# Performance work log

Measured on AMD Instinct MI355X. Metric: run time of the kernel, lower is better.

## Reference

```python
import jax, jax.numpy as jnp
import numpy as np

WH, WW = 7, 7
NUM_PRI = 3  # num_priorset=1 -> 3 prior tokens


def _rel_index():
    # Swin relative position index, extended with 3 prior-token columns.
    ch = np.arange(WH)
    cw = np.arange(WW)
    coords = np.stack(np.meshgrid(ch, cw, indexing='ij')).reshape(2, -1)  # [2, N]
    rel = coords[:, :, None] - coords[:, None, :]                          # [2, N, N]
    rel = rel.transpose(1, 2, 0).astype(np.int64)
    rel[..., 0] += WH - 1
    rel[..., 1] += WW - 1
    rel[..., 0] *= 2 * WW - 1
    idx = rel.sum(-1)                                                      # [N, N]
    N = WH * WW
    last = (2 * WH - 1) * (2 * WW - 1)  # 169
    full = np.full((N, N + NUM_PRI), last, dtype=np.int64)
    full[:, :N] = idx
    for j in range(NUM_PRI):
        full[:, N + j] = last + j
    return full

REL_IDX = jnp.asarray(_rel_index())  # [N, N+3]


def setup_inputs() -> dict:
    key = jax.random.key(0)
    ks = jax.random.split(key, 10)
    B, H, W, C = 8, 224, 224, 96
    nW = (H // WH) * (W // WW)  # 1024
    B_ = B * nW                  # 8192
    N = WH * WW                  # 49
    return {
        'x': jax.random.normal(ks[0], (B_, N, C), jnp.float32),
        'mask': jax.random.normal(ks[1], (nW, N, N), jnp.float32),
        'uk_prior': jax.random.normal(ks[2], (B, 1, C), jnp.float32),
        'fg_prior': jax.random.normal(ks[3], (B, 1, C), jnp.float32),
        'bg_prior': jax.random.normal(ks[4], (B, 1, C), jnp.float32),
        'qkv_w': jax.random.normal(ks[5], (3 * C, C), jnp.float32) * 0.02,
        'qkv_b': jax.random.normal(ks[6], (3 * C,), jnp.float32) * 0.02,
        'proj_w': jax.random.normal(ks[7], (C, C), jnp.float32) * 0.02,
        'proj_b': jax.random.normal(ks[8], (C,), jnp.float32) * 0.02,
        'bias_table': jax.random.normal(ks[9], (169 + NUM_PRI, 3), jnp.float32) * 0.02,
        'H': H,
        'W': W,
    }


def reference(x, mask, uk_prior, fg_prior, bg_prior, qkv_w, qkv_b, proj_w, proj_b, bias_table, H, W):
    B_, N, C = x.shape
    nH = bias_table.shape[1]
    hd = C // nH
    scale = hd ** (-0.5)
    nW = (H // WH) * (W // WW)
    B = B_ // nW

    prior_hw = jnp.concatenate([uk_prior, fg_prior, bg_prior], axis=1)  # [B, 3, C]
    # replicate the 3 priors into every window: [B, nW, 3, C] -> [B_, 3, C]
    pri = jnp.broadcast_to(prior_hw[:, None, :, :], (B, nW, NUM_PRI, C)).reshape(B_, NUM_PRI, C)
    x_ext = jnp.concatenate([x, pri], axis=1)                            # [B_, N+3, C]

    qkv = (x_ext @ qkv_w.T + qkv_b).reshape(B_, N + NUM_PRI, 3, nH, hd)
    qkv = qkv.transpose(2, 0, 3, 1, 4)                                   # [3, B_, nH, N+3, hd]
    q, k, v = qkv[0], qkv[1], qkv[2]
    q = q[:, :, :N, :] * scale                                           # [B_, nH, N, hd]

    attn = jnp.einsum('bhnd,bhmd->bhnm', q, k)                           # [B_, nH, N, N+3]
    bias = bias_table[REL_IDX]                                           # [N, N+3, nH]
    attn = attn + bias.transpose(2, 0, 1)[None]

    mask_p = jnp.pad(mask, ((0, 0), (0, 0), (0, NUM_PRI)))               # [nW, N, N+3]
    attn = attn.reshape(B, nW, nH, N, N + NUM_PRI) + mask_p[None, :, None]
    attn = jax.nn.softmax(attn.reshape(B_, nH, N, N + NUM_PRI), axis=-1)

    out = jnp.einsum('bhnm,bhmd->bnhd', attn, v).reshape(B_, N, C)
    out = out @ proj_w.T + proj_b

    # prior highway: run qkv on the raw priors, take v, project
    qkv_hw = (prior_hw @ qkv_w.T + qkv_b).reshape(B, NUM_PRI, 3, nH, hd)
    v_hw = qkv_hw[:, :, 2].reshape(B, NUM_PRI, C)
    v_hw = v_hw @ proj_w.T + proj_b
    return out, v_hw
```

## Files before the change

kernel.cpp:

```cpp
#include <hip/hip_runtime.h>
#include <hip/hip_bf16.h>


typedef __bf16 bf16x8 __attribute__((ext_vector_type(8)));
typedef float  f32x4  __attribute__((ext_vector_type(4)));
typedef short  s16x4  __attribute__((ext_vector_type(4)));
typedef unsigned short u16x4 __attribute__((ext_vector_type(4)));
using bf16 = __hip_bfloat16;

#define SCALE 0.17677669529663687f

#define LDS_XQ    0
#define LDS_K     4900
#define LDS_P     10100
#define LDS_VT    13432
#define LDS_TOT   19960

static __device__ inline float s2f(unsigned short s) {
    unsigned int u = ((unsigned int)s) << 16;
    float f;
    __builtin_memcpy(&f, &u, 4);
    return f;
}
static __device__ inline short f2s(float f) {
    __bf16 h = (__bf16)f;
    short s;
    __builtin_memcpy(&s, &h, 2);
    return s;
}
static __device__ inline bf16x8 ldw8(const float* p) {
    f32x4 a = *reinterpret_cast<const f32x4*>(p);
    f32x4 b = *reinterpret_cast<const f32x4*>(p + 4);
    bf16x8 r;
    #pragma unroll
    for (int i = 0; i < 4; ++i) {
        r[i]     = (__bf16)a[i];
        r[i + 4] = (__bf16)b[i];
    }
    return r;
}

__global__ __launch_bounds__(256)
void pawsa_prep(const float* __restrict__ qkv_w, const float* __restrict__ proj_w,
                const float* __restrict__ bias_table, bf16* __restrict__ ws)
{
    int blk = blockIdx.x, t = threadIdx.x;
    if (blk < 144) {
        int i = blk * 256 + t;
        if (i < 27648)      ws[i] = __float2bfloat16(qkv_w[i]);
        else if (i < 36864) ws[i] = __float2bfloat16(proj_w[i - 27648]);
        return;
    }
    int lane = t & 63, wid = t >> 6;
    int lr = lane & 15, lg = lane >> 4;
    u16x4* bg = reinterpret_cast<u16x4*>(ws + 36864);
    for (int h = 0; h < 3; ++h) {
        for (int nt = 0; nt < 4; ++nt) {
            int c = nt * 16 + lr;
            u16x4 v4;
            for (int j = 0; j < 4; ++j) {
                int n = wid * 16 + lg * 4 + j;
                int idx = 171;
                if (c < 49) {
                    idx = (n / 7 - c / 7 + 6) * 13 + ((n % 7) - (c % 7) + 6);
                    if (idx > 171 || idx < 0) idx = 171;
                } else if (c < 52) {
                    idx = 169 + (c - 49);
                }
                v4[j] = (unsigned short)f2s(bias_table[idx * 3 + h]);
            }
            bg[(h * 4 + nt) * 256 + t] = v4;
        }
    }
}

__global__ __launch_bounds__(256, 4)
void pawsa_main(const float* __restrict__ x, const float* __restrict__ mask,
                const float* __restrict__ uk, const float* __restrict__ fg,
                const float* __restrict__ bg,
                const bf16* __restrict__ wq,
                const float* __restrict__ qkv_b,
                const bf16* __restrict__ wp,
                const float* __restrict__ proj_b,
                const u16x4* __restrict__ biasg,
                float* __restrict__ out)
{
    __shared__ short smem[LDS_TOT];

    const int tid  = threadIdx.x;
    const int bid  = blockIdx.x;
    const int xcd  = bid & 7;
    const int slot = bid >> 3;
    const int wi   = xcd * 128 + (slot & 127);
    const int b    = slot >> 7;
    const int w    = b * 1024 + wi;

    const int lane = tid & 63;
    const int wid  = tid >> 6;
    const int lr   = lane & 15;
    const int lg   = lane >> 4;

    bf16x8 af[3][4];
    #pragma unroll
    for (int mt = 0; mt < 4; ++mt) {
        int n = mt * 16 + lr;
        #pragma unroll
        for (int ks = 0; ks < 3; ++ks) {
            bf16x8 a = (bf16x8)0;
            if (n < 49) {
                a = ldw8(x + ((size_t)w * 49 + n) * 96 + ks * 32 + lg * 8);
            } else if (n < 52) {
                const float* pr = (n == 49) ? uk : (n == 50) ? fg : bg;
                a = ldw8(pr + b * 96 + ks * 32 + lg * 8);
            }
            af[ks][mt] = a;
        }
    }

    const int nt0 = (wid < 3) ? wid * 5 : 13;
    #pragma unroll
    for (int i = 0; i < 5; ++i) {
        int nt = nt0 + i;
        bf16x8 bw0 = *reinterpret_cast<const bf16x8*>(wq + (nt * 16 + lr) * 96 +  0 + lg * 8);
        bf16x8 bw1 = *reinterpret_cast<const bf16x8*>(wq + (nt * 16 + lr) * 96 + 32 + lg * 8);
        bf16x8 bw2 = *reinterpret_cast<const bf16x8*>(wq + (nt * 16 + lr) * 96 + 64 + lg * 8);
        f32x4 qb4 = *reinterpret_cast<const f32x4*>(qkv_b + nt * 16 + lg * 4);
        f32x4 acc[4] = {(f32x4)0.f, (f32x4)0.f, (f32x4)0.f, (f32x4)0.f};
        #pragma unroll
        for (int mt = 0; mt < 4; ++mt) {
            acc[mt] = __builtin_amdgcn_mfma_f32_16x16x32_bf16(bw0, af[0][mt], acc[mt], 0, 0, 0);
            acc[mt] = __builtin_amdgcn_mfma_f32_16x16x32_bf16(bw1, af[1][mt], acc[mt], 0, 0, 0);
            acc[mt] = __builtin_amdgcn_mfma_f32_16x16x32_bf16(bw2, af[2][mt], acc[mt], 0, 0, 0);
        }
        int s = nt / 6;
        int remBase = (nt - s * 6) * 16 + lg * 4;
        #pragma unroll
        for (int mt = 0; mt < 4; ++mt) {
            int n = mt * 16 + lr;
            if (s == 2) {
                #pragma unroll
                for (int j = 0; j < 4; ++j)
                    smem[LDS_VT + (remBase + j) * 68 + n] = f2s(acc[mt][j] + qb4[j]);
            } else {
                s16x4 pk;
                #pragma unroll
                for (int j = 0; j < 4; ++j) pk[j] = f2s(acc[mt][j] + qb4[j]);
                if (s == 0) { if (n < 49) *reinterpret_cast<s16x4*>(
                                  &smem[LDS_XQ + n * 100 + remBase]) = pk; }
                else        { if (n < 52) *reinterpret_cast<s16x4*>(
                                  &smem[LDS_K  + n * 100 + remBase]) = pk; }
            }
        }
    }

    float mk[4][4];
    #pragma unroll
    for (int nt = 0; nt < 4; ++nt) {
        int c = nt * 16 + lr;
        #pragma unroll
        for (int j = 0; j < 4; ++j) {
            int n = wid * 16 + lg * 4 + j;
            float m = 0.f;
            if (c < 49 && n < 49)
                m = mask[(size_t)wi * 2401 + n * 49 + c];
            mk[nt][j] = m;
        }
    }
    u16x4 bgv[12];
    #pragma unroll
    for (int i = 0; i < 12; ++i) bgv[i] = biasg[i * 256 + tid];

    __syncthreads();

    #pragma unroll
    for (int h = 0; h < 3; ++h) {
        bf16x8 aq = *reinterpret_cast<const bf16x8*>(
            &smem[LDS_XQ + (wid * 16 + lr) * 100 + h * 32 + lg * 8]);
        f32x4 sacc[4];
        #pragma unroll
        for (int nt = 0; nt < 4; ++nt) {
            bf16x8 bk = *reinterpret_cast<const bf16x8*>(
                &smem[LDS_K + (nt * 16 + lr) * 100 + h * 32 + lg * 8]);
            sacc[nt] = __builtin_amdgcn_mfma_f32_16x16x32_bf16(aq, bk, (f32x4)0.f, 0, 0, 0);
        }
        float lgt[4][4];
        #pragma unroll
        for (int nt = 0; nt < 4; ++nt) {
            int c = nt * 16 + lr;
            u16x4 bgq = bgv[h * 4 + nt];
            #pragma unroll
            for (int j = 0; j < 4; ++j) {
                float v = -1e30f;
                if (c < 52)
                    v = sacc[nt][j] * SCALE + s2f(bgq[j]) + mk[nt][j];
                lgt[nt][j] = v;
            }
        }
        float pr[4][4];
        #pragma unroll
        for (int j = 0; j < 4; ++j) {
            float m = fmaxf(fmaxf(lgt[0][j], lgt[1][j]), fmaxf(lgt[2][j], lgt[3][j]));
            m = fmaxf(m, __shfl_xor(m, 1));
            m = fmaxf(m, __shfl_xor(m, 2));
            m = fmaxf(m, __shfl_xor(m, 4));
            m = fmaxf(m, __shfl_xor(m, 8));
            float sum = 0.f;
            #pragma unroll
            for (int nt = 0; nt < 4; ++nt) {
                pr[nt][j] = __expf(lgt[nt][j] - m);
                sum += pr[nt][j];
            }
            sum += __shfl_xor(sum, 1);
            sum += __shfl_xor(sum, 2);
            sum += __shfl_xor(sum, 4);
            sum += __shfl_xor(sum, 8);
            float inv = 1.0f / sum;
            #pragma unroll
            for (int nt = 0; nt < 4; ++nt) pr[nt][j] *= inv;
        }
        #pragma unroll
        for (int nt = 0; nt < 4; ++nt)
            #pragma unroll
            for (int j = 0; j < 4; ++j) {
                int prow = wid * 16 + lg * 4 + j;
                if (prow < 49)
                    smem[LDS_P + prow * 68 + nt * 16 + lr] = f2s(pr[nt][j]);
            }

        f32x4 ov[2] = {(f32x4)0.f, (f32x4)0.f};
        #pragma unroll
        for (int ks = 0; ks < 2; ++ks) {
            bf16x8 ap = *reinterpret_cast<const bf16x8*>(
                &smem[LDS_P + (wid * 16 + lr) * 68 + ks * 32 + lg * 8]);
            #pragma unroll
            for (int nt2 = 0; nt2 < 2; ++nt2) {
                bf16x8 bv = *reinterpret_cast<const bf16x8*>(
                    &smem[LDS_VT + (h * 32 + nt2 * 16 + lr) * 68 + ks * 32 + lg * 8]);
                ov[nt2] = __builtin_amdgcn_mfma_f32_16x16x32_bf16(ap, bv, ov[nt2], 0, 0, 0);
            }
        }
        #pragma unroll
        for (int nt2 = 0; nt2 < 2; ++nt2)
            #pragma unroll
            for (int j = 0; j < 4; ++j) {
                int orow = wid * 16 + lg * 4 + j;
                if (orow < 49)
                    smem[LDS_XQ + orow * 100 + h * 32 + nt2 * 16 + lr]
                        = f2s(ov[nt2][j]);
            }
    }

    f32x4 po[6];
    #pragma unroll
    for (int nt = 0; nt < 6; ++nt) po[nt] = (f32x4)0.f;
    #pragma unroll
    for (int ks = 0; ks < 3; ++ks) {
        bf16x8 a = *reinterpret_cast<const bf16x8*>(
            &smem[LDS_XQ + (wid * 16 + lr) * 100 + ks * 32 + lg * 8]);
        #pragma unroll
        for (int nt = 0; nt < 6; ++nt) {
            bf16x8 bp = *reinterpret_cast<const bf16x8*>(
                wp + (nt * 16 + lr) * 96 + ks * 32 + lg * 8);
            po[nt] = __builtin_amdgcn_mfma_f32_16x16x32_bf16(a, bp, po[nt], 0, 0, 0);
        }
    }
    #pragma unroll
    for (int nt = 0; nt < 6; ++nt) {
        float pb = proj_b[nt * 16 + lr];
        #pragma unroll
        for (int j = 0; j < 4; ++j) {
            int n = wid * 16 + lg * 4 + j;
            if (n < 49)
                out[((size_t)w * 49 + n) * 96 + nt * 16 + lr] = po[nt][j] + pb;
        }
    }
}

__global__ __launch_bounds__(128)
void pawsa_prior(const float* __restrict__ uk, const float* __restrict__ fg,
                 const float* __restrict__ bg,
                 const float* __restrict__ qkv_w, const float* __restrict__ qkv_b,
                 const float* __restrict__ proj_w, const float* __restrict__ proj_b,
                 float* __restrict__ out_vhw)
{
    int blk = blockIdx.x;
    int b = blk / 3, p = blk % 3;
    int t = threadIdx.x;
    __shared__ float prr[96], vf[96];
    const float* src = (p == 0) ? uk : (p == 1) ? fg : bg;
    if (t < 96) prr[t] = src[b * 96 + t];
    __syncthreads();
    if (t < 96) {
        float acc = qkv_b[192 + t];
        for (int k = 0; k < 96; ++k)
            acc += prr[k] * qkv_w[(192 + t) * 96 + k];
        vf[t] = acc;
    }
    __syncthreads();
    if (t < 96) {
        float acc = proj_b[t];
        for (int c = 0; c < 96; ++c)
            acc += vf[c] * proj_w[t * 96 + c];
        out_vhw[(b * 3 + p) * 96 + t] = acc;
    }
}

extern "C" void kernel_launch(void* const* d_in, const int* in_sizes, int n_in,
                              void* d_out, int out_size, void* d_ws, size_t ws_size,
                              hipStream_t stream) {
    const float* x          = (const float*)d_in[0];
    const float* mask       = (const float*)d_in[1];
    const float* uk         = (const float*)d_in[2];
    const float* fg         = (const float*)d_in[3];
    const float* bg         = (const float*)d_in[4];
    const float* qkv_w      = (const float*)d_in[5];
    const float* qkv_b      = (const float*)d_in[6];
    const float* proj_w     = (const float*)d_in[7];
    const float* proj_b     = (const float*)d_in[8];
    const float* bias_table = (const float*)d_in[9];
    float* out = (float*)d_out;
    bf16* ws   = (bf16*)d_ws;

    pawsa_prep<<<145, 256, 0, stream>>>(qkv_w, proj_w, bias_table, ws);
    pawsa_prior<<<24, 128, 0, stream>>>(uk, fg, bg, qkv_w, qkv_b, proj_w, proj_b,
                                        out + (size_t)8192 * 49 * 96);
    pawsa_main<<<8192, 256, 0, stream>>>(x, mask, uk, fg, bg,
                                         ws, qkv_b, ws + 27648, proj_b,
                                         (const u16x4*)(ws + 36864), out);
}
```

Measured before the change: 234.7 us.

## Process two windows per block to reuse weight fragments

Each block now handles two consecutive windows, so the per-block loads of QKV weight fragments, qkv bias, the relative-position bias and the projection weights are amortized over twice the work. LDS doubles to hold both windows' Q/K/P/V, launch bounds drop to 2 blocks per SM, and the grid halves. The XCD-aware window-to-block remap is dropped in favor of linear window indexing, which may change L2 locality for the mask reads. Register pressure rises from the doubled A fragments and accumulators.

```diff
diff --git a/kernel.cpp b/kernel.cpp
--- a/kernel.cpp
+++ b/kernel.cpp
@@ -14,7 +14,8 @@
 #define LDS_K     4900
 #define LDS_P     10100
 #define LDS_VT    13432
-#define LDS_TOT   19960
+#define WIN_SZ    19960
+#define LDS_TOT   39920
 
 static __device__ inline float s2f(unsigned short s) {
     unsigned int u = ((unsigned int)s) << 16;
@@ -74,7 +75,7 @@
     }
 }
 
-__global__ __launch_bounds__(256, 4)
+__global__ __launch_bounds__(256, 2)
 void pawsa_main(const float* __restrict__ x, const float* __restrict__ mask,
                 const float* __restrict__ uk, const float* __restrict__ fg,
                 const float* __restrict__ bg,
@@ -88,32 +89,30 @@
     __shared__ short smem[LDS_TOT];
 
     const int tid  = threadIdx.x;
-    const int bid  = blockIdx.x;
-    const int xcd  = bid & 7;
-    const int slot = bid >> 3;
-    const int wi   = xcd * 128 + (slot & 127);
-    const int b    = slot >> 7;
-    const int w    = b * 1024 + wi;
-
+    const int w0   = blockIdx.x * 2;
     const int lane = tid & 63;
     const int wid  = tid >> 6;
     const int lr   = lane & 15;
     const int lg   = lane >> 4;
 
-    bf16x8 af[3][4];
-    #pragma unroll
-    for (int mt = 0; mt < 4; ++mt) {
-        int n = mt * 16 + lr;
-        #pragma unroll
-        for (int ks = 0; ks < 3; ++ks) {
-            bf16x8 a = (bf16x8)0;
-            if (n < 49) {
-                a = ldw8(x + ((size_t)w * 49 + n) * 96 + ks * 32 + lg * 8);
-            } else if (n < 52) {
-                const float* pr = (n == 49) ? uk : (n == 50) ? fg : bg;
-                a = ldw8(pr + b * 96 + ks * 32 + lg * 8);
-            }
-            af[ks][mt] = a;
+    bf16x8 af[2][3][4];
+    #pragma unroll
+    for (int u = 0; u < 2; ++u) {
+        int w = w0 + u, b = w >> 10;
+        #pragma unroll
+        for (int mt = 0; mt < 4; ++mt) {
+            int n = mt * 16 + lr;
+            #pragma unroll
+            for (int ks = 0; ks < 3; ++ks) {
+                bf16x8 a = (bf16x8)0;
+                if (n < 49) {
+                    a = ldw8(x + ((size_t)w * 49 + n) * 96 + ks * 32 + lg * 8);
+                } else if (n < 52) {
+                    const float* pr = (n == 49) ? uk : (n == 50) ? fg : bg;
+                    a = ldw8(pr + b * 96 + ks * 32 + lg * 8);
+                }
+                af[u][ks][mt] = a;
+            }
         }
     }
 
@@ -125,153 +124,174 @@
         bf16x8 bw1 = *reinterpret_cast<const bf16x8*>(wq + (nt * 16 + lr) * 96 + 32 + lg * 8);
         bf16x8 bw2 = *reinterpret_cast<const bf16x8*>(wq + (nt * 16 + lr) * 96 + 64 + lg * 8);
         f32x4 qb4 = *reinterpret_cast<const f32x4*>(qkv_b + nt * 16 + lg * 4);
-        f32x4 acc[4] = {(f32x4)0.f, (f32x4)0.f, (f32x4)0.f, (f32x4)0.f};
-        #pragma unroll
-        for (int mt = 0; mt < 4; ++mt) {
-            acc[mt] = __builtin_amdgcn_mfma_f32_16x16x32_bf16(bw0, af[0][mt], acc[mt], 0, 0, 0);
-            acc[mt] = __builtin_amdgcn_mfma_f32_16x16x32_bf16(bw1, af[1][mt], acc[mt], 0, 0, 0);
-            acc[mt] = __builtin_amdgcn_mfma_f32_16x16x32_bf16(bw2, af[2][mt], acc[mt], 0, 0, 0);
-        }
         int s = nt / 6;
         int remBase = (nt - s * 6) * 16 + lg * 4;
         #pragma unroll
-        for (int mt = 0; mt < 4; ++mt) {
-            int n = mt * 16 + lr;
-            if (s == 2) {
-                #pragma unroll
-                for (int j = 0; j < 4; ++j)
-                    smem[LDS_VT + (remBase + j) * 68 + n] = f2s(acc[mt][j] + qb4[j]);
-            } else {
-                s16x4 pk;
-                #pragma unroll
-                for (int j = 0; j < 4; ++j) pk[j] = f2s(acc[mt][j] + qb4[j]);
-                if (s == 0) { if (n < 49) *reinterpret_cast<s16x4*>(
-                                  &smem[LDS_XQ + n * 100 + remBase]) = pk; }
-                else        { if (n < 52) *reinterpret_cast<s16x4*>(
-                                  &smem[LDS_K  + n * 100 + remBase]) = pk; }
-            }
-        }
-    }
-
-    float mk[4][4];
-    #pragma unroll
-    for (int nt = 0; nt < 4; ++nt) {
-        int c = nt * 16 + lr;
-        #pragma unroll
-        for (int j = 0; j < 4; ++j) {
-            int n = wid * 16 + lg * 4 + j;
-            float m = 0.f;
-            if (c < 49 && n < 49)
-                m = mask[(size_t)wi * 2401 + n * 49 + c];
-            mk[nt][j] = m;
-        }
-    }
-    u16x4 bgv[12];
-    #pragma unroll
-    for (int i = 0; i < 12; ++i) bgv[i] = biasg[i * 256 + tid];
-
-    __syncthreads();
-
-    #pragma unroll
-    for (int h = 0; h < 3; ++h) {
-        bf16x8 aq = *reinterpret_cast<const bf16x8*>(
-            &smem[LDS_XQ + (wid * 16 + lr) * 100 + h * 32 + lg * 8]);
-        f32x4 sacc[4];
-        #pragma unroll
-        for (int nt = 0; nt < 4; ++nt) {
-            bf16x8 bk = *reinterpret_cast<const bf16x8*>(
-                &smem[LDS_K + (nt * 16 + lr) * 100 + h * 32 + lg * 8]);
-            sacc[nt] = __builtin_amdgcn_mfma_f32_16x16x32_bf16(aq, bk, (f32x4)0.f, 0, 0, 0);
-        }
-        float lgt[4][4];
+        for (int u = 0; u < 2; ++u) {
+            const int WB = u * WIN_SZ;
+            f32x4 acc[4] = {(f32x4)0.f, (f32x4)0.f, (f32x4)0.f, (f32x4)0.f};
+            #pragma unroll
+            for (int mt = 0; mt < 4; ++mt) {
+                acc[mt] = __builtin_amdgcn_mfma_f32_16x16x32_bf16(bw0, af[u][0][mt], acc[mt], 0, 0, 0);
+                acc[mt] = __builtin_amdgcn_mfma_f32_16x16x32_bf16(bw1, af[u][1][mt], acc[mt], 0, 0, 0);
+                acc[mt] = __builtin_amdgcn_mfma_f32_16x16x32_bf16(bw2, af[u][2][mt], acc[mt], 0, 0, 0);
+            }
+            #pragma unroll
+            for (int mt = 0; mt < 4; ++mt) {
+                int n = mt * 16 + lr;
+                if (s == 2) {
+                    #pragma unroll
+                    for (int j = 0; j < 4; ++j)
+                        smem[WB + LDS_VT + (remBase + j) * 68 + n] = f2s(acc[mt][j] + qb4[j]);
+                } else {
+                    s16x4 pk;
+                    #pragma unroll
+                    for (int j = 0; j < 4; ++j) pk[j] = f2s(acc[mt][j] + qb4[j]);
+                    if (s == 0) { if (n < 49) *reinterpret_cast<s16x4*>(
+                                      &smem[WB + LDS_XQ + n * 100 + remBase]) = pk; }
+                    else        { if (n < 52) *reinterpret_cast<s16x4*>(
+                                      &smem[WB + LDS_K  + n * 100 + remBase]) = pk; }
+                }
+            }
+        }
+    }
+
+    float mk[2][4][4];
+    #pragma unroll
+    for (int u = 0; u < 2; ++u) {
+        int wiu = (w0 + u) & 1023;
         #pragma unroll
         for (int nt = 0; nt < 4; ++nt) {
             int c = nt * 16 + lr;
-            u16x4 bgq = bgv[h * 4 + nt];
             #pragma unroll
             for (int j = 0; j < 4; ++j) {
-                float v = -1e30f;
-                if (c < 52)
-                    v = sacc[nt][j] * SCALE + s2f(bgq[j]) + mk[nt][j];
-                lgt[nt][j] = v;
-            }
-        }
-        float pr[4][4];
-        #pragma unroll
-        for (int j = 0; j < 4; ++j) {
-            float m = fmaxf(fmaxf(lgt[0][j], lgt[1][j]), fmaxf(lgt[2][j], lgt[3][j]));
-            m = fmaxf(m, __shfl_xor(m, 1));
-            m = fmaxf(m, __shfl_xor(m, 2));
-            m = fmaxf(m, __shfl_xor(m, 4));
-            m = fmaxf(m, __shfl_xor(m, 8));
-            float sum = 0.f;
+                int n = wid * 16 + lg * 4 + j;
+                float m = 0.f;
+                if (c < 49 && n < 49)
+                    m = mask[(size_t)wiu * 2401 + n * 49 + c];
+                mk[u][nt][j] = m;
+            }
+        }
+    }
+    u16x4 bgv[12];
+    #pragma unroll
+    for (int i = 0; i < 12; ++i) bgv[i] = biasg[i * 256 + tid];
+
+    __syncthreads();
+
+    #pragma unroll
+    for (int h = 0; h < 3; ++h) {
+        #pragma unroll
+        for (int u = 0; u < 2; ++u) {
+            const int WB = u * WIN_SZ;
+            bf16x8 aq = *reinterpret_cast<const bf16x8*>(
+                &smem[WB + LDS_XQ + (wid * 16 + lr) * 100 + h * 32 + lg * 8]);
+            f32x4 sacc[4];
             #pragma unroll
             for (int nt = 0; nt < 4; ++nt) {
-                pr[nt][j] = __expf(lgt[nt][j] - m);
-                sum += pr[nt][j];
-            }
-            sum += __shfl_xor(sum, 1);
-            sum += __shfl_xor(sum, 2);
-            sum += __shfl_xor(sum, 4);
-            sum += __shfl_xor(sum, 8);
-            float inv = 1.0f / sum;
-            #pragma unroll
-            for (int nt = 0; nt < 4; ++nt) pr[nt][j] *= inv;
-        }
-        #pragma unroll
-        for (int nt = 0; nt < 4; ++nt)
+                bf16x8 bk = *reinterpret_cast<const bf16x8*>(
+                    &smem[WB + LDS_K + (nt * 16 + lr) * 100 + h * 32 + lg * 8]);
+                sacc[nt] = __builtin_amdgcn_mfma_f32_16x16x32_bf16(aq, bk, (f32x4)0.f, 0, 0, 0);
+            }
+            float lgt[4][4];
+            #pragma unroll
+            for (int nt = 0; nt < 4; ++nt) {
+                int c = nt * 16 + lr;
+                u16x4 bgq = bgv[h * 4 + nt];
+                #pragma unroll
+                for (int j = 0; j < 4; ++j) {
+                    float v = -1e30f;
+                    if (c < 52)
+                        v = sacc[nt][j] * SCALE + s2f(bgq[j]) + mk[u][nt][j];
+                    lgt[nt][j] = v;
+                }
+            }
+            float pr[4][4];
             #pragma unroll
             for (int j = 0; j < 4; ++j) {
-                int prow = wid * 16 + lg * 4 + j;
-                if (prow < 49)
-                    smem[LDS_P + prow * 68 + nt * 16 + lr] = f2s(pr[nt][j]);
-            }
-
-        f32x4 ov[2] = {(f32x4)0.f, (f32x4)0.f};
-        #pragma unroll
-        for (int ks = 0; ks < 2; ++ks) {
-            bf16x8 ap = *reinterpret_cast<const bf16x8*>(
-                &smem[LDS_P + (wid * 16 + lr) * 68 + ks * 32 + lg * 8]);
-            #pragma unroll
-            for (int nt2 = 0; nt2 < 2; ++nt2) {
-                bf16x8 bv = *reinterpret_cast<const bf16x8*>(
-                    &smem[LDS_VT + (h * 32 + nt2 * 16 + lr) * 68 + ks * 32 + lg * 8]);
-                ov[nt2] = __builtin_amdgcn_mfma_f32_16x16x32_bf16(ap, bv, ov[nt2], 0, 0, 0);
-            }
-        }
-        #pragma unroll
-        for (int nt2 = 0; nt2 < 2; ++nt2)
-            #pragma unroll
-            for (int j = 0; j < 4; ++j) {
-                int orow = wid * 16 + lg * 4 + j;
-                if (orow < 49)
-                    smem[LDS_XQ + orow * 100 + h * 32 + nt2 * 16 + lr]
-                        = f2s(ov[nt2][j]);
-            }
-    }
-
-    f32x4 po[6];
-    #pragma unroll
-    for (int nt = 0; nt < 6; ++nt) po[nt] = (f32x4)0.f;
+                float m = fmaxf(fmaxf(lgt[0][j], lgt[1][j]), fmaxf(lgt[2][j], lgt[3][j]));
+                m = fmaxf(m, __shfl_xor(m, 1));
+                m = fmaxf(m, __shfl_xor(m, 2));
+                m = fmaxf(m, __shfl_xor(m, 4));
+                m = fmaxf(m, __shfl_xor(m, 8));
+                float sum = 0.f;
+                #pragma unroll
+                for (int nt = 0; nt < 4; ++nt) {
+                    pr[nt][j] = __expf(lgt[nt][j] - m);
+                    sum += pr[nt][j];
+                }
+                sum += __shfl_xor(sum, 1);
+                sum += __shfl_xor(sum, 2);
+                sum += __shfl_xor(sum, 4);
+                sum += __shfl_xor(sum, 8);
+                float inv = 1.0f / sum;
+                #pragma unroll
+                for (int nt = 0; nt < 4; ++nt) pr[nt][j] *= inv;
+            }
+            #pragma unroll
+            for (int nt = 0; nt < 4; ++nt)
+                #pragma unroll
+                for (int j = 0; j < 4; ++j) {
+                    int prow = wid * 16 + lg * 4 + j;
+                    if (prow < 49)
+                        smem[WB + LDS_P + prow * 68 + nt * 16 + lr] = f2s(pr[nt][j]);
+                }
+
+            f32x4 ov[2] = {(f32x4)0.f, (f32x4)0.f};
+            #pragma unroll
+            for (int ks = 0; ks < 2; ++ks) {
+                bf16x8 ap = *reinterpret_cast<const bf16x8*>(
+                    &smem[WB + LDS_P + (wid * 16 + lr) * 68 + ks * 32 + lg * 8]);
+                #pragma unroll
+                for (int nt2 = 0; nt2 < 2; ++nt2) {
+                    bf16x8 bv = *reinterpret_cast<const bf16x8*>(
+                        &smem[WB + LDS_VT + (h * 32 + nt2 * 16 + lr) * 68 + ks * 32 + lg * 8]);
+                    ov[nt2] = __builtin_amdgcn_mfma_f32_16x16x32_bf16(ap, bv, ov[nt2], 0, 0, 0);
+                }
+            }
+            #pragma unroll
+            for (int nt2 = 0; nt2 < 2; ++nt2)
+                #pragma unroll
+                for (int j = 0; j < 4; ++j) {
+                    int orow = wid * 16 + lg * 4 + j;
+                    if (orow < 49)
+                        smem[WB + LDS_XQ + orow * 100 + h * 32 + nt2 * 16 + lr]
+                            = f2s(ov[nt2][j]);
+                }
+        }
+    }
+
+    f32x4 po[2][6];
+    #pragma unroll
+    for (int u = 0; u < 2; ++u)
+        #pragma unroll
+        for (int nt = 0; nt < 6; ++nt) po[u][nt] = (f32x4)0.f;
     #pragma unroll
     for (int ks = 0; ks < 3; ++ks) {
-        bf16x8 a = *reinterpret_cast<const bf16x8*>(
-            &smem[LDS_XQ + (wid * 16 + lr) * 100 + ks * 32 + lg * 8]);
+        bf16x8 a0 = *reinterpret_cast<const bf16x8*>(
+            &smem[0 * WIN_SZ + LDS_XQ + (wid * 16 + lr) * 100 + ks * 32 + lg * 8]);
+        bf16x8 a1 = *reinterpret_cast<const bf16x8*>(
+            &smem[1 * WIN_SZ + LDS_XQ + (wid * 16 + lr) * 100 + ks * 32 + lg * 8]);
         #pragma unroll
         for (int nt = 0; nt < 6; ++nt) {
             bf16x8 bp = *reinterpret_cast<const bf16x8*>(
                 wp + (nt * 16 + lr) * 96 + ks * 32 + lg * 8);
-            po[nt] = __builtin_amdgcn_mfma_f32_16x16x32_bf16(a, bp, po[nt], 0, 0, 0);
+            po[0][nt] = __builtin_amdgcn_mfma_f32_16x16x32_bf16(a0, bp, po[0][nt], 0, 0, 0);
+            po[1][nt] = __builtin_amdgcn_mfma_f32_16x16x32_bf16(a1, bp, po[1][nt], 0, 0, 0);
         }
     }
     #pragma unroll
     for (int nt = 0; nt < 6; ++nt) {
         float pb = proj_b[nt * 16 + lr];
         #pragma unroll
-        for (int j = 0; j < 4; ++j) {
-            int n = wid * 16 + lg * 4 + j;
-            if (n < 49)
-                out[((size_t)w * 49 + n) * 96 + nt * 16 + lr] = po[nt][j] + pb;
+        for (int u = 0; u < 2; ++u) {
+            size_t wbase = (size_t)(w0 + u) * 49;
+            #pragma unroll
+            for (int j = 0; j < 4; ++j) {
+                int n = wid * 16 + lg * 4 + j;
+                if (n < 49)
+                    out[(wbase + n) * 96 + nt * 16 + lr] = po[u][nt][j] + pb;
+            }
         }
     }
 }
@@ -324,7 +344,7 @@
     pawsa_prep<<<145, 256, 0, stream>>>(qkv_w, proj_w, bias_table, ws);
     pawsa_prior<<<24, 128, 0, stream>>>(uk, fg, bg, qkv_w, qkv_b, proj_w, proj_b,
                                         out + (size_t)8192 * 49 * 96);
-    pawsa_main<<<8192, 256, 0, stream>>>(x, mask, uk, fg, bg,
+    pawsa_main<<<4096, 256, 0, stream>>>(x, mask, uk, fg, bg,
                                          ws, qkv_b, ws + 27648, proj_b,
                                          (const u16x4*)(ws + 36864), out);
 }
```

New measurement: 294.0 us. +25.2%, slower.
